# Optimization experiments

Hardware: AMD Instinct MI355X
Metric: run time of the kernel (lower is better)

Reference implementation:

```python
import jax, jax.numpy as jnp
import numpy as np

N_NODES = 50000
N_EDGES = 800000
D_IN, D_HID, D_OUT = 128, 128, 64


def setup_inputs() -> dict:
    key = jax.random.key(0)
    ks = jax.random.split(key, 8)
    x = jax.random.normal(ks[0], (N_NODES, D_IN), dtype=jnp.float32)
    edge_index = jax.random.randint(ks[1], (2, N_EDGES), 0, N_NODES, dtype=jnp.int64)

    def glorot(k, shape):
        fan_in, fan_out = shape
        lim = jnp.sqrt(6.0 / (fan_in + fan_out)).astype(jnp.float32)
        return jax.random.uniform(k, shape, jnp.float32, -lim, lim)

    return {
        "x": x,
        "edge_index": edge_index,
        "W1": glorot(ks[2], (D_IN, D_HID)),
        "b1": jnp.zeros((D_HID,), jnp.float32),
        "W2": glorot(ks[3], (D_HID, D_HID)),
        "b2": jnp.zeros((D_HID,), jnp.float32),
        "W3": glorot(ks[4], (D_HID, D_OUT)),
        "b3": jnp.zeros((D_OUT,), jnp.float32),
    }


def reference(x, edge_index, W1, b1, W2, b2, W3, b3):
    # PyG GCNConv with normalize=False: h = x @ W, then sum-aggregate source
    # features onto targets (edge_index[0]=src, edge_index[1]=dst), add bias.
    src = edge_index[0]
    dst = edge_index[1]
    n = x.shape[0]

    def gcn_layer(h, W, b):
        hw = h @ W                      # [N, d_out] dense GEMM
        msg = hw[src]                   # [E, d_out] gather
        agg = jax.ops.segment_sum(msg, dst, num_segments=n)  # [N, d_out] scatter-add
        return agg + b

    o1 = gcn_layer(x, W1, b1)
    o2 = gcn_layer(o1, W2, b2)
    o3 = gcn_layer(o2, W3, b3)
    return (o1, o2, o3)
```

## Files before the change

### kernel.cpp

```cpp
#include <hip/hip_runtime.h>

#define N_NODES 50000
#define N_EDGES 800000
#define CAP 64

typedef unsigned int uint32;
typedef unsigned short u16;

typedef __attribute__((ext_vector_type(8))) short bf16x8;
typedef __attribute__((ext_vector_type(4))) float f32x4;

__device__ __forceinline__ uint32 f32_to_bf16_rne(float f) {
    uint32 u = __float_as_uint(f);
    u += 0x7fffu + ((u >> 16) & 1u);
    return u >> 16;
}
__device__ __forceinline__ float bf16lo_to_f32(uint32 v) { return __uint_as_float(v << 16); }
__device__ __forceinline__ float bf16hi_to_f32(uint32 v) { return __uint_as_float(v & 0xffff0000u); }

__global__ __launch_bounds__(256) void prep_kernel(const float* __restrict__ W1,
                                                   const float* __restrict__ W2,
                                                   const float* __restrict__ W3,
                                                   uint32* __restrict__ wt1,
                                                   uint32* __restrict__ wt2,
                                                   uint32* __restrict__ wt3,
                                                   int* __restrict__ cursor) {
    int b = blockIdx.x, tid = threadIdx.x;
    if (b < 196) {
        int i = b * 256 + tid;
        if (i < N_NODES) cursor[i] = 0;
        return;
    }
    b -= 196;
    const float* W;
    uint32* WT;
    int N;
    if (b < 32) { W = W1; WT = wt1; N = 128; }
    else if (b < 64) { W = W2; WT = wt2; N = 128; b -= 32; }
    else { W = W3; WT = wt3; N = 64; b -= 64; }
    int i = b * 256 + tid;
    if (i >= N * 64) return;
    int n = i >> 6, p = i & 63;
    WT[n * 64 + p] = f32_to_bf16_rne(W[(2 * p) * N + n]) |
                     (f32_to_bf16_rne(W[(2 * p + 1) * N + n]) << 16);
}

__device__ __forceinline__ void pack_store(uint32* __restrict__ Cb, int rowstride_u,
                                           int row, int col, int r16, float v) {
    float nb = __shfl_xor(v, 1);
    if ((r16 & 1) == 0) {
        uint32 p = f32_to_bf16_rne(v) | (f32_to_bf16_rne(nb) << 16);
        Cb[(size_t)row * rowstride_u + (col >> 1)] = p;
    }
}

__device__ __forceinline__ void gemm1_body(const float* __restrict__ A,
                                           const uint32* __restrict__ WTb,
                                           uint32* __restrict__ Cb, int M, int bid) {
    constexpr int NT = 2;
    const int tid = threadIdx.x;
    const int wave = tid >> 6;
    const int lane = tid & 63;
    const int r16 = lane & 15;
    const int g = lane >> 4;
    const int row0 = bid * 64;

    const float4* A4 = reinterpret_cast<const float4*>(A);
    const uint4* B4 = reinterpret_cast<const uint4*>(WTb);

    f32x4 acc[4][NT];
#pragma unroll
    for (int m = 0; m < 4; m++)
#pragma unroll
        for (int nt = 0; nt < NT; nt++) acc[m][nt] = (f32x4){0.f, 0.f, 0.f, 0.f};

    int rowm[4];
#pragma unroll
    for (int m = 0; m < 4; m++) {
        int r = row0 + m * 16 + r16;
        rowm[m] = r < M ? r : M - 1;
    }
    union U { uint4 u; bf16x8 v; };
#pragma unroll
    for (int kt = 0; kt < 4; kt++) {
        U b[NT];
#pragma unroll
        for (int nt = 0; nt < NT; nt++)
            b[nt].u = B4[(size_t)(nt * 64 + wave * 16 + r16) * 16 + kt * 4 + g];
        U a[4];
#pragma unroll
        for (int m = 0; m < 4; m++) {
            float4 f0 = A4[(size_t)rowm[m] * 32 + kt * 8 + g * 2];
            float4 f1 = A4[(size_t)rowm[m] * 32 + kt * 8 + g * 2 + 1];
            a[m].u.x = f32_to_bf16_rne(f0.x) | (f32_to_bf16_rne(f0.y) << 16);
            a[m].u.y = f32_to_bf16_rne(f0.z) | (f32_to_bf16_rne(f0.w) << 16);
            a[m].u.z = f32_to_bf16_rne(f1.x) | (f32_to_bf16_rne(f1.y) << 16);
            a[m].u.w = f32_to_bf16_rne(f1.z) | (f32_to_bf16_rne(f1.w) << 16);
        }
#pragma unroll
        for (int m = 0; m < 4; m++)
#pragma unroll
            for (int nt = 0; nt < NT; nt++)
                acc[m][nt] = __builtin_amdgcn_mfma_f32_16x16x32_bf16(a[m].v, b[nt].v, acc[m][nt], 0, 0, 0);
    }
#pragma unroll
    for (int m = 0; m < 4; m++)
#pragma unroll
        for (int nt = 0; nt < NT; nt++)
#pragma unroll
            for (int r = 0; r < 4; r++) {
                int row = row0 + m * 16 + g * 4 + r;
                if (row < M)
                    pack_store(Cb, 64, row, nt * 64 + wave * 16 + r16, r16, acc[m][nt][r]);
            }
}

#define EPT 8
#define EPB (256 * EPT)
#define GEMM1_BLOCKS 782
#define BUILD_CHUNKS 391

__global__ __launch_bounds__(256) void build_gemm1_kernel(const float* __restrict__ x,
                                                          const uint32* __restrict__ wt1,
                                                          uint32* __restrict__ hwb,
                                                          const int* __restrict__ ei,
                                                          int* __restrict__ cursor,
                                                          u16* __restrict__ adj) {
    if (blockIdx.x < GEMM1_BLOCKS) {
        gemm1_body(x, wt1, hwb, N_NODES, blockIdx.x);
        return;
    }
    const int bb = blockIdx.x - GEMM1_BLOCKS;
    const int part = bb & 7;
    const int chunk = bb >> 3;
    const int base = chunk * EPB + threadIdx.x * EPT;
#pragma unroll
    for (int i = 0; i < EPT; i += 4) {
        int e = base + i;
        if (e + 3 < N_EDGES) {
            int4 s4 = *reinterpret_cast<const int4*>(&ei[e]);
            int4 d4 = *reinterpret_cast<const int4*>(&ei[N_EDGES + e]);
            int ss[4] = {s4.x, s4.y, s4.z, s4.w};
            int dd[4] = {d4.x, d4.y, d4.z, d4.w};
#pragma unroll
            for (int j = 0; j < 4; j++) {
                int d = dd[j];
                if (((d >> 4) & 7) == part && (unsigned)d < (unsigned)N_NODES) {
                    int s = ss[j];
                    if ((unsigned)s >= (unsigned)N_NODES) s = 0;
                    int pos = atomicAdd(&cursor[d], 1);
                    if (pos < CAP) adj[d * CAP + pos] = (u16)s;
                }
            }
        } else {
            for (int j = 0; j < 4; j++) {
                int ee = e + j;
                if (ee < N_EDGES) {
                    int d = ei[N_EDGES + ee];
                    if (((d >> 4) & 7) == part && (unsigned)d < (unsigned)N_NODES) {
                        int s = ei[ee];
                        if ((unsigned)s >= (unsigned)N_NODES) s = 0;
                        int pos = atomicAdd(&cursor[d], 1);
                        if (pos < CAP) adj[d * CAP + pos] = (u16)s;
                    }
                }
            }
        }
    }
}

__device__ __forceinline__ void gather_q128(const uint32* __restrict__ sbase,
                                            int myslot, int d, int j, float a[8]) {
    int e = 0;
    for (; e + 16 <= d; e += 16) {
        int s0 = __shfl(myslot, e + j);
        int s1 = __shfl(myslot, e + 4 + j);
        int s2 = __shfl(myslot, e + 8 + j);
        int s3 = __shfl(myslot, e + 12 + j);
        uint4 v0 = *reinterpret_cast<const uint4*>(sbase + (size_t)s0 * 64);
        uint4 v1 = *reinterpret_cast<const uint4*>(sbase + (size_t)s1 * 64);
        uint4 v2 = *reinterpret_cast<const uint4*>(sbase + (size_t)s2 * 64);
        uint4 v3 = *reinterpret_cast<const uint4*>(sbase + (size_t)s3 * 64);
        a[0] += (bf16lo_to_f32(v0.x) + bf16lo_to_f32(v1.x)) + (bf16lo_to_f32(v2.x) + bf16lo_to_f32(v3.x));
        a[1] += (bf16hi_to_f32(v0.x) + bf16hi_to_f32(v1.x)) + (bf16hi_to_f32(v2.x) + bf16hi_to_f32(v3.x));
        a[2] += (bf16lo_to_f32(v0.y) + bf16lo_to_f32(v1.y)) + (bf16lo_to_f32(v2.y) + bf16lo_to_f32(v3.y));
        a[3] += (bf16hi_to_f32(v0.y) + bf16hi_to_f32(v1.y)) + (bf16hi_to_f32(v2.y) + bf16hi_to_f32(v3.y));
        a[4] += (bf16lo_to_f32(v0.z) + bf16lo_to_f32(v1.z)) + (bf16lo_to_f32(v2.z) + bf16lo_to_f32(v3.z));
        a[5] += (bf16hi_to_f32(v0.z) + bf16hi_to_f32(v1.z)) + (bf16hi_to_f32(v2.z) + bf16hi_to_f32(v3.z));
        a[6] += (bf16lo_to_f32(v0.w) + bf16lo_to_f32(v1.w)) + (bf16lo_to_f32(v2.w) + bf16lo_to_f32(v3.w));
        a[7] += (bf16hi_to_f32(v0.w) + bf16hi_to_f32(v1.w)) + (bf16hi_to_f32(v2.w) + bf16hi_to_f32(v3.w));
    }
    for (; e < d; e += 4) {
        int idx = e + j;
        int s = __shfl(myslot, idx < d ? idx : e);
        uint4 v = make_uint4(0u, 0u, 0u, 0u);
        if (idx < d) v = *reinterpret_cast<const uint4*>(sbase + (size_t)s * 64);
        a[0] += bf16lo_to_f32(v.x); a[1] += bf16hi_to_f32(v.x);
        a[2] += bf16lo_to_f32(v.y); a[3] += bf16hi_to_f32(v.y);
        a[4] += bf16lo_to_f32(v.z); a[5] += bf16hi_to_f32(v.z);
        a[6] += bf16lo_to_f32(v.w); a[7] += bf16hi_to_f32(v.w);
    }
}

template <int N>
__global__ __launch_bounds__(256) void agg_gemm_kernel(const uint32* __restrict__ hw_in,
                                                       const u16* __restrict__ adj,
                                                       const int* __restrict__ deg,
                                                       const float* __restrict__ bias,
                                                       float* __restrict__ o_out,
                                                       const uint32* __restrict__ WTb,
                                                       uint32* __restrict__ hw_out) {
    constexpr int TPW = N / 64;
    constexpr int LDR = 68;
    __shared__ uint32 Asm[16 * LDR];

    const int tid = threadIdx.x;
    const int wave = tid >> 6;
    const int lane = tid & 63;
    const int f = lane & 15;
    const int j = lane >> 4;
    const int base = blockIdx.x * 16;
    const uint32* sbase = hw_in + f * 4;

#pragma unroll
    for (int i = 0; i < 4; i++) {
        int n = base + wave * 4 + i;
        int d = __builtin_amdgcn_readfirstlane(deg[n]);
        if (d > CAP) d = CAP;
        int myslot = adj[n * CAP + lane];
        float a[8] = {0.f, 0.f, 0.f, 0.f, 0.f, 0.f, 0.f, 0.f};
        gather_q128(sbase, myslot, d, j, a);
#pragma unroll
        for (int off = 16; off < 64; off <<= 1)
#pragma unroll
            for (int k = 0; k < 8; k++) a[k] += __shfl_xor(a[k], off);
        if (lane < 16) {
            float4 b0 = *reinterpret_cast<const float4*>(&bias[f * 8]);
            float4 b1 = *reinterpret_cast<const float4*>(&bias[f * 8 + 4]);
            a[0] += b0.x; a[1] += b0.y; a[2] += b0.z; a[3] += b0.w;
            a[4] += b1.x; a[5] += b1.y; a[6] += b1.z; a[7] += b1.w;
            *reinterpret_cast<float4*>(&o_out[(size_t)n * 128 + f * 8]) =
                make_float4(a[0], a[1], a[2], a[3]);
            *reinterpret_cast<float4*>(&o_out[(size_t)n * 128 + f * 8 + 4]) =
                make_float4(a[4], a[5], a[6], a[7]);
            uint4 p;
            p.x = f32_to_bf16_rne(a[0]) | (f32_to_bf16_rne(a[1]) << 16);
            p.y = f32_to_bf16_rne(a[2]) | (f32_to_bf16_rne(a[3]) << 16);
            p.z = f32_to_bf16_rne(a[4]) | (f32_to_bf16_rne(a[5]) << 16);
            p.w = f32_to_bf16_rne(a[6]) | (f32_to_bf16_rne(a[7]) << 16);
            *reinterpret_cast<uint4*>(&Asm[(wave * 4 + i) * LDR + f * 4]) = p;
        }
    }
    __syncthreads();

    const int r16 = lane & 15;
    const int g = lane >> 4;
    const uint4* B4 = reinterpret_cast<const uint4*>(WTb);

    f32x4 acc[TPW];
#pragma unroll
    for (int nt = 0; nt < TPW; nt++) acc[nt] = (f32x4){0.f, 0.f, 0.f, 0.f};

    union U { uint4 u; bf16x8 v; };
#pragma unroll
    for (int kt = 0; kt < 4; kt++) {
        U a;
        a.u = *reinterpret_cast<const uint4*>(&Asm[r16 * LDR + (kt * 4 + g) * 4]);
        U b[TPW];
#pragma unroll
        for (int nt = 0; nt < TPW; nt++) {
            int col = (wave * TPW + nt) * 16 + r16;
            b[nt].u = B4[(size_t)col * 16 + kt * 4 + g];
        }
#pragma unroll
        for (int nt = 0; nt < TPW; nt++)
            acc[nt] = __builtin_amdgcn_mfma_f32_16x16x32_bf16(a.v, b[nt].v, acc[nt], 0, 0, 0);
    }
#pragma unroll
    for (int nt = 0; nt < TPW; nt++)
#pragma unroll
        for (int r = 0; r < 4; r++) {
            int row = base + g * 4 + r;
            pack_store(hw_out, N / 2, row, (wave * TPW + nt) * 16 + r16, r16, acc[nt][r]);
        }
}

__global__ __launch_bounds__(256) void aggregate64_kernel(const uint32* __restrict__ hwb,
                                                          const u16* __restrict__ adj,
                                                          const int* __restrict__ deg,
                                                          const float* __restrict__ bias,
                                                          float* __restrict__ out) {
    int n = (blockIdx.x * blockDim.x + threadIdx.x) >> 6;
    if (n >= N_NODES) return;
    const int lane = threadIdx.x & 63;
    const int f = lane & 7;
    const int j = lane >> 3;
    int d = __builtin_amdgcn_readfirstlane(deg[n]);
    if (d > CAP) d = CAP;
    int myslot = adj[n * CAP + lane];
    const uint32* sbase = hwb + f * 4;

    float a[8] = {0.f, 0.f, 0.f, 0.f, 0.f, 0.f, 0.f, 0.f};
    int e = 0;
    for (; e + 16 <= d; e += 16) {
        int s0 = __shfl(myslot, e + j);
        int s1 = __shfl(myslot, e + 8 + j);
        uint4 v0 = *reinterpret_cast<const uint4*>(sbase + (size_t)s0 * 32);
        uint4 v1 = *reinterpret_cast<const uint4*>(sbase + (size_t)s1 * 32);
        a[0] += bf16lo_to_f32(v0.x) + bf16lo_to_f32(v1.x);
        a[1] += bf16hi_to_f32(v0.x) + bf16hi_to_f32(v1.x);
        a[2] += bf16lo_to_f32(v0.y) + bf16lo_to_f32(v1.y);
        a[3] += bf16hi_to_f32(v0.y) + bf16hi_to_f32(v1.y);
        a[4] += bf16lo_to_f32(v0.z) + bf16lo_to_f32(v1.z);
        a[5] += bf16hi_to_f32(v0.z) + bf16hi_to_f32(v1.z);
        a[6] += bf16lo_to_f32(v0.w) + bf16lo_to_f32(v1.w);
        a[7] += bf16hi_to_f32(v0.w) + bf16hi_to_f32(v1.w);
    }
    for (; e < d; e += 8) {
        int idx = e + j;
        int s = __shfl(myslot, idx < d ? idx : e);
        uint4 v = make_uint4(0u, 0u, 0u, 0u);
        if (idx < d) v = *reinterpret_cast<const uint4*>(sbase + (size_t)s * 32);
        a[0] += bf16lo_to_f32(v.x); a[1] += bf16hi_to_f32(v.x);
        a[2] += bf16lo_to_f32(v.y); a[3] += bf16hi_to_f32(v.y);
        a[4] += bf16lo_to_f32(v.z); a[5] += bf16hi_to_f32(v.z);
        a[6] += bf16lo_to_f32(v.w); a[7] += bf16hi_to_f32(v.w);
    }
#pragma unroll
    for (int off = 8; off < 64; off <<= 1)
#pragma unroll
        for (int k = 0; k < 8; k++) a[k] += __shfl_xor(a[k], off);
    if (lane < 8) {
        float4 b0 = *reinterpret_cast<const float4*>(&bias[f * 8]);
        float4 b1 = *reinterpret_cast<const float4*>(&bias[f * 8 + 4]);
        *reinterpret_cast<float4*>(&out[(size_t)n * 64 + f * 8]) =
            make_float4(a[0] + b0.x, a[1] + b0.y, a[2] + b0.z, a[3] + b0.w);
        *reinterpret_cast<float4*>(&out[(size_t)n * 64 + f * 8 + 4]) =
            make_float4(a[4] + b1.x, a[5] + b1.y, a[6] + b1.z, a[7] + b1.w);
    }
}

extern "C" void kernel_launch(void* const* d_in, const int* in_sizes, int n_in,
                              void* d_out, int out_size, void* d_ws, size_t ws_size,
                              hipStream_t stream) {
    const float* x  = (const float*)d_in[0];
    const int*   ei = (const int*)d_in[1];
    const float* W1 = (const float*)d_in[2];
    const float* b1 = (const float*)d_in[3];
    const float* W2 = (const float*)d_in[4];
    const float* b2 = (const float*)d_in[5];
    const float* W3 = (const float*)d_in[6];
    const float* b3 = (const float*)d_in[7];

    float* o1 = (float*)d_out;
    float* o2 = o1 + (size_t)N_NODES * 128;
    float* o3 = o2 + (size_t)N_NODES * 128;

    char* ws = (char*)d_ws;
    uint32* hwbA   = (uint32*)(ws);
    uint32* hwbB   = (uint32*)(ws + 12800000);
    u16*    adj    = (u16*)(ws + 25600000);
    int*    cursor = (int*)(ws + 32000000);
    uint32* wt1    = (uint32*)(ws + 32200000);
    uint32* wt2    = (uint32*)(ws + 32232768);
    uint32* wt3    = (uint32*)(ws + 32265536);

    prep_kernel<<<276, 256, 0, stream>>>(W1, W2, W3, wt1, wt2, wt3, cursor);
    build_gemm1_kernel<<<GEMM1_BLOCKS + BUILD_CHUNKS * 8, 256, 0, stream>>>(x, wt1, hwbA, ei, cursor, adj);
    agg_gemm_kernel<128><<<3125, 256, 0, stream>>>(hwbA, adj, cursor, b1, o1, wt2, hwbB);
    agg_gemm_kernel<64><<<3125, 256, 0, stream>>>(hwbB, adj, cursor, b2, o2, wt3, hwbA);
    aggregate64_kernel<<<12500, 256, 0, stream>>>(hwbA, adj, cursor, b3, o3);
}
```

Before: 163.0 us.

## Build adjacency via two-level bucket scatter with shared-memory atomics

Replaces direct per-node global atomics for building the CSR-like adjacency with a two-pass scheme. Edges are first binned into 128-node buckets using a shared-memory histogram and one global atomic per bucket per block. A second kernel then places each bucket's edges into per-node slots with shared-memory atomics. This removes the 8x re-reading of edges across partitions and most global atomic contention, at the cost of an extra kernel launch, an intermediate buffer, and a fixed bucket capacity that could overflow on skewed graphs.

```diff
diff --git a/kernel.cpp b/kernel.cpp
--- a/kernel.cpp
+++ b/kernel.cpp
@@ -3,6 +3,8 @@
 #define N_NODES 50000
 #define N_EDGES 800000
 #define CAP 64
+#define NBUCK 391
+#define BCAP 3072
 
 typedef unsigned int uint32;
 typedef unsigned short u16;
@@ -24,14 +26,14 @@
                                                    uint32* __restrict__ wt1,
                                                    uint32* __restrict__ wt2,
                                                    uint32* __restrict__ wt3,
-                                                   int* __restrict__ cursor) {
+                                                   uint32* __restrict__ bcursor) {
     int b = blockIdx.x, tid = threadIdx.x;
-    if (b < 196) {
+    if (b < 2) {
         int i = b * 256 + tid;
-        if (i < N_NODES) cursor[i] = 0;
+        if (i < NBUCK) bcursor[i] = 0;
         return;
     }
-    b -= 196;
+    b -= 2;
     const float* W;
     uint32* WT;
     int N;
@@ -115,57 +117,83 @@
             }
 }
 
-#define EPT 8
-#define EPB (256 * EPT)
 #define GEMM1_BLOCKS 782
-#define BUILD_CHUNKS 391
-
-__global__ __launch_bounds__(256) void build_gemm1_kernel(const float* __restrict__ x,
-                                                          const uint32* __restrict__ wt1,
-                                                          uint32* __restrict__ hwb,
-                                                          const int* __restrict__ ei,
-                                                          int* __restrict__ cursor,
-                                                          u16* __restrict__ adj) {
+#define SCAT_BLOCKS 391
+
+__global__ __launch_bounds__(256) void scatter_gemm1_kernel(const float* __restrict__ x,
+                                                            const uint32* __restrict__ wt1,
+                                                            uint32* __restrict__ hwb,
+                                                            const int* __restrict__ ei,
+                                                            uint32* __restrict__ bcursor,
+                                                            uint32* __restrict__ bedges) {
     if (blockIdx.x < GEMM1_BLOCKS) {
         gemm1_body(x, wt1, hwb, N_NODES, blockIdx.x);
         return;
     }
-    const int bb = blockIdx.x - GEMM1_BLOCKS;
-    const int part = bb & 7;
-    const int chunk = bb >> 3;
-    const int base = chunk * EPB + threadIdx.x * EPT;
-#pragma unroll
-    for (int i = 0; i < EPT; i += 4) {
-        int e = base + i;
-        if (e + 3 < N_EDGES) {
-            int4 s4 = *reinterpret_cast<const int4*>(&ei[e]);
-            int4 d4 = *reinterpret_cast<const int4*>(&ei[N_EDGES + e]);
-            int ss[4] = {s4.x, s4.y, s4.z, s4.w};
-            int dd[4] = {d4.x, d4.y, d4.z, d4.w};
-#pragma unroll
-            for (int j = 0; j < 4; j++) {
-                int d = dd[j];
-                if (((d >> 4) & 7) == part && (unsigned)d < (unsigned)N_NODES) {
-                    int s = ss[j];
-                    if ((unsigned)s >= (unsigned)N_NODES) s = 0;
-                    int pos = atomicAdd(&cursor[d], 1);
-                    if (pos < CAP) adj[d * CAP + pos] = (u16)s;
-                }
+    const int chunk = blockIdx.x - GEMM1_BLOCKS;
+    __shared__ uint32 hist[NBUCK];
+    const int tid = threadIdx.x;
+    for (int t = tid; t < NBUCK; t += 256) hist[t] = 0;
+    __syncthreads();
+
+    uint32 meta[8], payload[8];
+    const int base = chunk * 2048;
+#pragma unroll
+    for (int k = 0; k < 8; k++) {
+        int e = base + k * 256 + tid;
+        meta[k] = 0xFFFFFFFFu;
+        if (e < N_EDGES) {
+            int s = ei[e];
+            int dt = ei[N_EDGES + e];
+            if ((unsigned)dt < (unsigned)N_NODES) {
+                if ((unsigned)s >= (unsigned)N_NODES) s = 0;
+                int b = dt >> 7;
+                uint32 slot = atomicAdd(&hist[b], 1u);
+                meta[k] = (uint32)b | (slot << 9);
+                payload[k] = (uint32)s | ((uint32)(dt & 127) << 16);
             }
-        } else {
-            for (int j = 0; j < 4; j++) {
-                int ee = e + j;
-                if (ee < N_EDGES) {
-                    int d = ei[N_EDGES + ee];
-                    if (((d >> 4) & 7) == part && (unsigned)d < (unsigned)N_NODES) {
-                        int s = ei[ee];
-                        if ((unsigned)s >= (unsigned)N_NODES) s = 0;
-                        int pos = atomicAdd(&cursor[d], 1);
-                        if (pos < CAP) adj[d * CAP + pos] = (u16)s;
-                    }
-                }
-            }
-        }
+        }
+    }
+    __syncthreads();
+    for (int t = tid; t < NBUCK; t += 256) {
+        uint32 h = hist[t];
+        uint32 g = h ? atomicAdd(&bcursor[t], h) : 0u;
+        hist[t] = g;
+    }
+    __syncthreads();
+#pragma unroll
+    for (int k = 0; k < 8; k++) {
+        if (meta[k] != 0xFFFFFFFFu) {
+            uint32 b = meta[k] & 511u;
+            uint32 addr = hist[b] + (meta[k] >> 9);
+            if (addr < BCAP) bedges[(size_t)b * BCAP + addr] = payload[k];
+        }
+    }
+}
+
+__global__ __launch_bounds__(256) void bucket_build_kernel(const uint32* __restrict__ bedges,
+                                                           const uint32* __restrict__ bcursor,
+                                                           u16* __restrict__ adj,
+                                                           int* __restrict__ deg) {
+    const int b = blockIdx.x;
+    __shared__ uint32 cur[128];
+    const int tid = threadIdx.x;
+    if (tid < 128) cur[tid] = 0;
+    __syncthreads();
+    uint32 cnt = bcursor[b];
+    if (cnt > BCAP) cnt = BCAP;
+    const uint32* be = bedges + (size_t)b * BCAP;
+    for (uint32 i = tid; i < cnt; i += 256) {
+        uint32 p = be[i];
+        uint32 dl = p >> 16;
+        uint32 s = p & 0xFFFFu;
+        uint32 pos = atomicAdd(&cur[dl], 1u);
+        if (pos < CAP) adj[((size_t)(b * 128 + dl)) * CAP + pos] = (u16)s;
+    }
+    __syncthreads();
+    if (tid < 128) {
+        int n = b * 128 + tid;
+        if (n < N_NODES) deg[n] = (int)cur[tid];
     }
 }
 
@@ -357,17 +385,20 @@
     float* o3 = o2 + (size_t)N_NODES * 128;
 
     char* ws = (char*)d_ws;
-    uint32* hwbA   = (uint32*)(ws);
-    uint32* hwbB   = (uint32*)(ws + 12800000);
-    u16*    adj    = (u16*)(ws + 25600000);
-    int*    cursor = (int*)(ws + 32000000);
-    uint32* wt1    = (uint32*)(ws + 32200000);
-    uint32* wt2    = (uint32*)(ws + 32232768);
-    uint32* wt3    = (uint32*)(ws + 32265536);
-
-    prep_kernel<<<276, 256, 0, stream>>>(W1, W2, W3, wt1, wt2, wt3, cursor);
-    build_gemm1_kernel<<<GEMM1_BLOCKS + BUILD_CHUNKS * 8, 256, 0, stream>>>(x, wt1, hwbA, ei, cursor, adj);
-    agg_gemm_kernel<128><<<3125, 256, 0, stream>>>(hwbA, adj, cursor, b1, o1, wt2, hwbB);
-    agg_gemm_kernel<64><<<3125, 256, 0, stream>>>(hwbB, adj, cursor, b2, o2, wt3, hwbA);
-    aggregate64_kernel<<<12500, 256, 0, stream>>>(hwbA, adj, cursor, b3, o3);
-}
+    uint32* hwbA    = (uint32*)(ws);
+    uint32* hwbB    = (uint32*)(ws + 12800000);
+    u16*    adj     = (u16*)(ws + 25600000);
+    int*    deg     = (int*)(ws + 32000000);
+    uint32* bedges  = (uint32*)(ws + 32200000);
+    uint32* bcursor = (uint32*)(ws + 37004608);
+    uint32* wt1     = (uint32*)(ws + 37006464);
+    uint32* wt2     = (uint32*)(ws + 37039232);
+    uint32* wt3     = (uint32*)(ws + 37072000);
+
+    prep_kernel<<<82, 256, 0, stream>>>(W1, W2, W3, wt1, wt2, wt3, bcursor);
+    scatter_gemm1_kernel<<<GEMM1_BLOCKS + SCAT_BLOCKS, 256, 0, stream>>>(x, wt1, hwbA, ei, bcursor, bedges);
+    bucket_build_kernel<<<NBUCK, 256, 0, stream>>>(bedges, bcursor, adj, deg);
+    agg_gemm_kernel<128><<<3125, 256, 0, stream>>>(hwbA, adj, deg, b1, o1, wt2, hwbB);
+    agg_gemm_kernel<64><<<3125, 256, 0, stream>>>(hwbB, adj, deg, b2, o2, wt3, hwbA);
+    aggregate64_kernel<<<12500, 256, 0, stream>>>(hwbA, adj, deg, b3, o3);
+}
```

New measurement: 146.0 us. 1.12x faster.
